# Kernel tuning notes

Measured on AMD Instinct MI355X. Metric: run time of the kernel, lower is better.

Reference implementation:

```python
import jax, jax.numpy as jnp
import numpy as np

N_NODES = 100000
DROP_P = 0.1


def gcn_conv(x, W, b, row, col, n_nodes):
    """PyG GCNConv: out = D^{-1/2}(A+I)D^{-1/2} X W + b.
    row/col already include self-loops. Messages flow row(src) -> col(dst)."""
    xw = x @ W  # [N, H]
    deg = jax.ops.segment_sum(jnp.ones_like(col, dtype=xw.dtype), col, num_segments=n_nodes)
    dinv = jnp.where(deg > 0, jax.lax.rsqrt(deg), 0.0)
    norm = dinv[row] * dinv[col]  # [E]
    msg = norm[:, None] * xw[row]  # [E, H] gather + scale
    out = jax.ops.segment_sum(msg, col, num_segments=n_nodes)  # scatter-add
    return out + b


def dropout(x, key, p):
    keep = jax.random.bernoulli(key, 1.0 - p, x.shape)
    return jnp.where(keep, x / (1.0 - p), 0.0).astype(x.dtype)


def prelu(x, alpha):
    return jnp.where(x >= 0, x, alpha[None, :] * x)


def setup_inputs() -> dict:
    key = jax.random.key(0)
    k1, k2, k3, k4 = jax.random.split(key, 4)
    in_ch, hid = 128, 128
    n_edges = 1600000
    x = jax.random.normal(k1, (N_NODES, in_ch), dtype=jnp.float32)
    edge_index = jax.random.randint(k2, (2, n_edges), 0, N_NODES, dtype=jnp.int64)
    s = 1.0 / np.sqrt(in_ch)
    W1 = jax.random.normal(k3, (in_ch, hid), dtype=jnp.float32) * s
    W2 = jax.random.normal(k4, (hid, hid), dtype=jnp.float32) * s
    b1 = jnp.zeros((hid,), dtype=jnp.float32)
    b2 = jnp.zeros((hid,), dtype=jnp.float32)
    alpha = jnp.full((hid,), 0.25, dtype=jnp.float32)
    return {"x": x, "edge_index": edge_index, "W1": W1, "b1": b1,
            "W2": W2, "b2": b2, "alpha": alpha}


def reference(x, edge_index, W1, b1, W2, b2, alpha):
    n = x.shape[0]
    # add self-loops once (PyG default add_self_loops=True)
    loop = jnp.arange(n, dtype=edge_index.dtype)
    row = jnp.concatenate([edge_index[0], loop])
    col = jnp.concatenate([edge_index[1], loop])

    dk1, dk2 = jax.random.split(jax.random.key(42))
    h = gcn_conv(x, W1, b1, row, col, n)
    h = dropout(h, dk1, DROP_P)
    h = prelu(h, alpha)
    h = gcn_conv(h, W2, b2, row, col, n)
    h = dropout(h, dk2, DROP_P)
    h = prelu(h, alpha)
    return h
```

## Files before the change

kernel.cpp:

```cpp
#include <hip/hip_runtime.h>
#include <stdint.h>
#include <string.h>

__host__ __device__ inline uint32_t rotl32(uint32_t x, int r) {
    return (x << r) | (x >> (32 - r));
}

__host__ __device__ inline void tf2x32(uint32_t k0, uint32_t k1,
                                       uint32_t x0, uint32_t x1,
                                       uint32_t& o0, uint32_t& o1) {
    uint32_t ks0 = k0, ks1 = k1, ks2 = k0 ^ k1 ^ 0x1BD11BDAu;
    x0 += ks0; x1 += ks1;
#define TF_R4(a,b,c,d) \
    x0 += x1; x1 = rotl32(x1,a); x1 ^= x0; \
    x0 += x1; x1 = rotl32(x1,b); x1 ^= x0; \
    x0 += x1; x1 = rotl32(x1,c); x1 ^= x0; \
    x0 += x1; x1 = rotl32(x1,d); x1 ^= x0;
    TF_R4(13,15,26,6)  x0 += ks1; x1 += ks2 + 1u;
    TF_R4(17,29,16,24) x0 += ks2; x1 += ks0 + 2u;
    TF_R4(13,15,26,6)  x0 += ks0; x1 += ks1 + 3u;
    TF_R4(17,29,16,24) x0 += ks1; x1 += ks2 + 4u;
    TF_R4(13,15,26,6)  x0 += ks2; x1 += ks0 + 5u;
#undef TF_R4
    o0 = x0; o1 = x1;
}

__device__ inline unsigned pk2h(float a, float b) {
    _Float16 ha = (_Float16)a, hb = (_Float16)b;
    unsigned short ua, ub;
    __builtin_memcpy(&ua, &ha, 2);
    __builtin_memcpy(&ub, &hb, 2);
    return (unsigned)ua | ((unsigned)ub << 16);
}
__device__ inline unsigned short h16bits(float a) {
    _Float16 h = (_Float16)a;
    unsigned short u; __builtin_memcpy(&u, &h, 2);
    return u;
}
__device__ inline float lo16(unsigned u) {
    unsigned short s = (unsigned short)(u & 0xffffu);
    _Float16 h; __builtin_memcpy(&h, &s, 2);
    return (float)h;
}
__device__ inline float hi16(unsigned u) {
    unsigned short s = (unsigned short)(u >> 16);
    _Float16 h; __builtin_memcpy(&h, &s, 2);
    return (float)h;
}

typedef float fx4 __attribute__((ext_vector_type(4)));
typedef unsigned ux4 __attribute__((ext_vector_type(4)));
typedef _Float16 h16x8 __attribute__((ext_vector_type(8)));
typedef _Float16 h16x2 __attribute__((ext_vector_type(2)));
typedef float f32x4 __attribute__((ext_vector_type(4)));

__device__ inline h16x2 as_h2(unsigned u) { h16x2 r; __builtin_memcpy(&r, &u, 4); return r; }

#define CSR_CAP 48
#define NBKT 256
#define PART_EPB 8192

__global__ __launch_bounds__(256) void k_part(
        const int* __restrict__ ei, long long* __restrict__ gbkt,
        unsigned* __restrict__ gbcnt,
        unsigned long long* __restrict__ m1, unsigned long long* __restrict__ m2,
        const float* __restrict__ x, unsigned* __restrict__ xb,
        const float* __restrict__ w1, const float* __restrict__ w2,
        _Float16* __restrict__ wt1, _Float16* __restrict__ wt2,
        unsigned k1a, unsigned k1b, unsigned k2a, unsigned k2b,
        int E, int N, int bw, int bcap, int total,
        int PB, int MB, int CB) {
    __shared__ unsigned hcnt[NBKT], hoff[NBKT], hrun[NBKT];
    int b = blockIdx.x;
    int t = (int)threadIdx.x;
    if (b < PB) {
        int base = b * PART_EPB;
        hcnt[t] = 0; hrun[t] = 0;
        __syncthreads();
        for (int i = 0; i < PART_EPB / 256; ++i) {
            int e = base + i * 256 + t;
            if (e < E) {
                int c = __builtin_nontemporal_load(ei + (size_t)E + e);
                int r = __builtin_nontemporal_load(ei + e);
                if ((unsigned)c < (unsigned)N && (unsigned)r < (unsigned)N)
                    atomicAdd(&hcnt[(unsigned)c / (unsigned)bw], 1u);
            }
        }
        __syncthreads();
        hoff[t] = atomicAdd(&gbcnt[t], hcnt[t]);
        __syncthreads();
        for (int i = 0; i < PART_EPB / 256; ++i) {
            int e = base + i * 256 + t;
            if (e < E) {
                int c = ei[(size_t)E + e];
                int r = ei[e];
                if ((unsigned)c < (unsigned)N && (unsigned)r < (unsigned)N) {
                    unsigned sp = (unsigned)c / (unsigned)bw;
                    unsigned rank = atomicAdd(&hrun[sp], 1u);
                    unsigned gp = hoff[sp] + rank;
                    if (gp < (unsigned)bcap)
                        gbkt[(size_t)sp * bcap + gp] =
                            (long long)(unsigned)r | ((long long)(unsigned)c << 32);
                }
            }
        }
        return;
    }
    b -= PB;
    if (b < MB) {
        int wv = (b * 256 + t) >> 6;
        int lane = t & 63;
        int TW = (2 * total) >> 6;
        int half = total >> 6;
        int w0 = wv * 8;
#pragma unroll
        for (int j = 0; j < 8; j++) {
            int wd = w0 + j;
            if (wd < TW) {
                int wl = wd;
                unsigned ka = k1a, kb = k1b;
                unsigned long long* m = m1;
                if (wl >= half) { wl -= half; ka = k2a; kb = k2b; m = m2; }
                uint32_t o0, o1;
                tf2x32(ka, kb, 0u, (uint32_t)(wl * 64 + lane), o0, o1);
                bool keep = (((o0 ^ o1) >> 9) < 7549747u);
                unsigned long long bal = __ballot(keep);
                if (lane == 0)
                    __builtin_nontemporal_store(bal, m + wl);
            }
        }
        return;
    }
    b -= MB;
    if (b < CB) {
        int i = b * 256 + t;
        if (i < (total >> 3)) {
            const fx4* src = (const fx4*)(x + (size_t)i * 8);
            fx4 a = __builtin_nontemporal_load(src);
            fx4 bb = __builtin_nontemporal_load(src + 1);
            ux4 v;
            v.x = pk2h(a.x, a.y);
            v.y = pk2h(a.z, a.w);
            v.z = pk2h(bb.x, bb.y);
            v.w = pk2h(bb.z, bb.w);
            __builtin_nontemporal_store(v, (ux4*)xb + i);
        }
        return;
    }
    b -= CB;
    int idx = b * 256 + t;
    int mat = idx >> 14;
    int e2 = idx & 16383;
    int c = e2 >> 7, k = e2 & 127;
    const float* W = mat ? w2 : w1;
    _Float16* WT = mat ? wt2 : wt1;
    WT[(size_t)c * 128 + k] = (_Float16)W[(size_t)k * 128 + c];
}

__global__ __launch_bounds__(256) void k_work(
        const long long* __restrict__ gbkt, const unsigned* __restrict__ gbcnt,
        unsigned* __restrict__ cnt, unsigned* __restrict__ csr,
        float* __restrict__ dinv, uint4* __restrict__ xb4,
        int N, int bw, int bcap) {
    __shared__ unsigned lcnt[512];
    int b = blockIdx.x;
    int t = (int)threadIdx.x;
    int lo = b * bw;
    int hi = lo + bw; if (hi > N) hi = N;
    int w = hi - lo; if (w < 0) w = 0;
    lcnt[t] = 0; lcnt[t + 256] = 0;
    __syncthreads();
    unsigned ne = gbcnt[b];
    if (ne > (unsigned)bcap) ne = (unsigned)bcap;
    const long long* base = gbkt + (size_t)b * bcap;
    for (unsigned e = t; e < ne; e += 256) {
        long long v = __builtin_nontemporal_load(base + e);
        unsigned r = (unsigned)(v & 0xffffffffll);
        unsigned c = (unsigned)(v >> 32);
        unsigned slot = atomicAdd(&lcnt[c - (unsigned)lo], 1u);
        if (slot < (unsigned)CSR_CAP)
            csr[(size_t)c * CSR_CAP + slot] = r;
    }
    __syncthreads();
    for (int i = t; i < w; i += 256)
        cnt[lo + i] = lcnt[i];
    for (int idx = t; idx < w * 16; idx += 256) {
        int nl = idx >> 4, part = idx & 15;
        int node = lo + nl;
        float d = rsqrtf((float)lcnt[nl] + 1.0f);
        if (part == 0) dinv[node] = d;
        uint4 u = xb4[(size_t)node * 16 + part];
        uint4 o;
        o.x = pk2h(d * lo16(u.x), d * hi16(u.x));
        o.y = pk2h(d * lo16(u.y), d * hi16(u.y));
        o.z = pk2h(d * lo16(u.z), d * hi16(u.z));
        o.w = pk2h(d * lo16(u.w), d * hi16(u.w));
        xb4[(size_t)node * 16 + part] = o;
    }
}

template <int OUT_HALF>
__global__ __launch_bounds__(128, 8) void k_layer(
        const unsigned short* __restrict__ in,
        const _Float16* __restrict__ WT,
        const float* __restrict__ bias, const float* __restrict__ alpha,
        const unsigned long long* __restrict__ mask,
        const float* __restrict__ dinv, const unsigned* __restrict__ cnt,
        const unsigned* __restrict__ csr,
        void* outv, int n) {
    __shared__ unsigned hls[32 * 68];
    int t = (int)threadIdx.x;
    int wv = t >> 6;
    int l = t & 63;
    int rowbase = blockIdx.x * 32 + wv * 16;
    unsigned* hl = hls + wv * 16 * 68;
    int slot = l >> 4;
    int lm = l & 15;
    int ci = lm << 3;

    int prow = rowbase + lm;
    bool pv = prow < n;
    float dnAll = pv ? dinv[prow] : 0.f;
    unsigned cAll = pv ? cnt[prow] : 0u;
    if (cAll > (unsigned)CSR_CAP) cAll = (unsigned)CSR_CAP;

#pragma unroll
    for (int g = 0; g < 4; ++g) {
        int rloc = g * 4 + slot;
        int node = rowbase + rloc;
        float dn = __shfl(dnAll, rloc);
        unsigned ecnt = (unsigned)__shfl((int)cAll, rloc);
        h16x2 a0 = (h16x2)0, a1 = (h16x2)0, a2 = (h16x2)0, a3 = (h16x2)0;
        size_t eb = (size_t)node * CSR_CAP;
        unsigned e = 0;
        unsigned nb4 = ecnt >> 2;
#pragma unroll 2
        for (unsigned bb = 0; bb < nb4; ++bb) {
            ux4 rr = __builtin_nontemporal_load((const ux4*)(csr + eb + e));
            uint4 u0 = *(const uint4*)(in + ((size_t)rr.x << 7) + ci);
            uint4 u1 = *(const uint4*)(in + ((size_t)rr.y << 7) + ci);
            uint4 u2 = *(const uint4*)(in + ((size_t)rr.z << 7) + ci);
            uint4 u3 = *(const uint4*)(in + ((size_t)rr.w << 7) + ci);
            a0 += as_h2(u0.x); a1 += as_h2(u0.y); a2 += as_h2(u0.z); a3 += as_h2(u0.w);
            a0 += as_h2(u1.x); a1 += as_h2(u1.y); a2 += as_h2(u1.z); a3 += as_h2(u1.w);
            a0 += as_h2(u2.x); a1 += as_h2(u2.y); a2 += as_h2(u2.z); a3 += as_h2(u2.w);
            a0 += as_h2(u3.x); a1 += as_h2(u3.y); a2 += as_h2(u3.z); a3 += as_h2(u3.w);
            e += 4;
        }
        for (; e < ecnt; ++e) {
            unsigned r0 = csr[eb + e];
            uint4 u0 = *(const uint4*)(in + ((size_t)r0 << 7) + ci);
            a0 += as_h2(u0.x); a1 += as_h2(u0.y); a2 += as_h2(u0.z); a3 += as_h2(u0.w);
        }
        if (node < n) {
            uint4 sv = *(const uint4*)(in + ((size_t)node << 7) + ci);
            a0 += as_h2(sv.x); a1 += as_h2(sv.y); a2 += as_h2(sv.z); a3 += as_h2(sv.w);
        }
        uint4 o;
        o.x = pk2h(dn * (float)a0[0], dn * (float)a0[1]);
        o.y = pk2h(dn * (float)a1[0], dn * (float)a1[1]);
        o.z = pk2h(dn * (float)a2[0], dn * (float)a2[1]);
        o.w = pk2h(dn * (float)a3[0], dn * (float)a3[1]);
        *(uint4*)(hl + (size_t)rloc * 68 + lm * 4) = o;
    }

    int kq = l >> 4;
    h16x8 afr[4];
#pragma unroll
    for (int kk = 0; kk < 4; kk++)
        afr[kk] = *(const h16x8*)(hl + (size_t)lm * 68 + kq * 4 + kk * 16);
#pragma unroll
    for (int f = 0; f < 8; f++) {
        f32x4 acc = (f32x4){0.f, 0.f, 0.f, 0.f};
#pragma unroll
        for (int kk = 0; kk < 4; kk++) {
            h16x8 bfr = *(const h16x8*)(WT + (size_t)(f * 16 + lm) * 128 + kk * 32 + kq * 8);
            acc = __builtin_amdgcn_mfma_f32_16x16x32_f16(afr[kk], bfr, acc, 0, 0, 0);
        }
        int c = f * 16 + lm;
        float bs = bias[c];
        float al = alpha[c];
#pragma unroll
        for (int j = 0; j < 4; j++) {
            int rl = kq * 4 + j;
            int rg = rowbase + rl;
            if (rg < n) {
                unsigned long long wmw = mask[((size_t)rg << 1) + (f >> 2)];
                bool keep = (wmw >> (c & 63)) & 1ull;
                float v = acc[j] + bs;
                v = keep ? v * (1.0f / 0.9f) : 0.0f;
                v = (v >= 0.f) ? v : al * v;
                if (OUT_HALF) {
                    float dnrow = __shfl(dnAll, rl);
                    __builtin_nontemporal_store(h16bits(v * dnrow),
                        (unsigned short*)outv + (size_t)rg * 128 + c);
                } else {
                    __builtin_nontemporal_store(v,
                        (float*)outv + (size_t)rg * 128 + c);
                }
            }
        }
    }
}

extern "C" void kernel_launch(void* const* d_in, const int* in_sizes, int n_in,
                              void* d_out, int out_size, void* d_ws, size_t ws_size,
                              hipStream_t stream) {
    const float* x  = (const float*)d_in[0];
    const int*   ei = (const int*)d_in[1];
    const float* W1 = (const float*)d_in[2];
    const float* b1 = (const float*)d_in[3];
    const float* W2 = (const float*)d_in[4];
    const float* b2 = (const float*)d_in[5];
    const float* al = (const float*)d_in[6];
    int N = in_sizes[0] / 128;
    int E = in_sizes[1] / 2;
    float* out = (float*)d_out;

    int bw = (N + NBKT - 1) / NBKT;
    int bcap = E / NBKT + E / NBKT / 4 + 1024;

    char* p = (char*)d_ws;
    unsigned short* xb = (unsigned short*)p;   p += (size_t)N * 128 * 2;
    unsigned short* ab = (unsigned short*)p;   p += (size_t)N * 128 * 2;
    long long* gbkt = (long long*)ab;
    unsigned* cnt = (unsigned*)p;              p += (size_t)N * 4;
    float* dinv = (float*)p;                   p += (size_t)N * 4;
    unsigned* csr = (unsigned*)p;              p += (size_t)N * CSR_CAP * 4;
    unsigned long long* m1 = (unsigned long long*)p;  p += ((size_t)N * 128 / 64) * 8;
    unsigned long long* m2 = (unsigned long long*)p;  p += ((size_t)N * 128 / 64) * 8;
    _Float16* wt1 = (_Float16*)p;              p += 128 * 128 * 2;
    _Float16* wt2 = (_Float16*)p;              p += 128 * 128 * 2;
    unsigned* gbcnt = (unsigned*)p;

    hipMemsetAsync(gbcnt, 0, NBKT * 4, stream);

    uint32_t dk1a, dk1b, dk2a, dk2b;
    tf2x32(0u, 42u, 0u, 0u, dk1a, dk1b);
    tf2x32(0u, 42u, 0u, 1u, dk2a, dk2b);

    int total = N * 128;
    int PB = (E + PART_EPB - 1) / PART_EPB;
    int TW = (2 * total) / 64;
    int MB = (TW + 31) / 32;
    int CB = (total / 8 + 255) / 256;
    int WB = (2 * 128 * 128 + 255) / 256;
    k_part<<<PB + MB + CB + WB, 256, 0, stream>>>(ei, gbkt, gbcnt, m1, m2,
                                                  x, (unsigned*)xb,
                                                  W1, W2, wt1, wt2,
                                                  dk1a, dk1b, dk2a, dk2b,
                                                  E, N, bw, bcap, total,
                                                  PB, MB, CB);
    k_work<<<NBKT, 256, 0, stream>>>(gbkt, gbcnt, cnt, csr, dinv, (uint4*)xb,
                                     N, bw, bcap);

    int LB = (N + 31) / 32;
    k_layer<1><<<LB, 128, 0, stream>>>(xb, wt1, b1, al, m1, dinv, cnt, csr, ab, N);
    k_layer<0><<<LB, 128, 0, stream>>>(ab, wt2, b2, al, m2, dinv, cnt, csr, out, N);
}
```

Measured before the change: 299.4 us.

## Split feature channels across both waves per 16-row block in layer kernel

Each block now handles 16 rows instead of 32, and its two waves split the 128 channels in half. Each lane gathers 8-byte chunks instead of 16-byte ones, and each wave computes 4 of the 8 MFMA output column tiles after a block-wide barrier. The change doubles the grid size and spreads the gather work across more blocks, which may improve latency hiding and load balance. In exchange, every CSR index is read twice (once per wave), the gather loads are narrower, and a __syncthreads is added.

Result: slower. 317.0 us (+5.9%).

```diff
diff --git a/kernel.cpp b/kernel.cpp
--- a/kernel.cpp
+++ b/kernel.cpp
@@ -208,15 +208,14 @@
         const float* __restrict__ dinv, const unsigned* __restrict__ cnt,
         const unsigned* __restrict__ csr,
         void* outv, int n) {
-    __shared__ unsigned hls[32 * 68];
+    __shared__ unsigned hl[16 * 68];
     int t = (int)threadIdx.x;
     int wv = t >> 6;
     int l = t & 63;
-    int rowbase = blockIdx.x * 32 + wv * 16;
-    unsigned* hl = hls + wv * 16 * 68;
+    int rowbase = blockIdx.x * 16;
     int slot = l >> 4;
     int lm = l & 15;
-    int ci = lm << 3;
+    int ch = wv * 64 + lm * 4;
 
     int prow = rowbase + lm;
     bool pv = prow < n;
@@ -230,39 +229,39 @@
         int node = rowbase + rloc;
         float dn = __shfl(dnAll, rloc);
         unsigned ecnt = (unsigned)__shfl((int)cAll, rloc);
-        h16x2 a0 = (h16x2)0, a1 = (h16x2)0, a2 = (h16x2)0, a3 = (h16x2)0;
+        h16x2 a0 = (h16x2)0, a1 = (h16x2)0;
         size_t eb = (size_t)node * CSR_CAP;
         unsigned e = 0;
         unsigned nb4 = ecnt >> 2;
 #pragma unroll 2
         for (unsigned bb = 0; bb < nb4; ++bb) {
             ux4 rr = __builtin_nontemporal_load((const ux4*)(csr + eb + e));
-            uint4 u0 = *(const uint4*)(in + ((size_t)rr.x << 7) + ci);
-            uint4 u1 = *(const uint4*)(in + ((size_t)rr.y << 7) + ci);
-            uint4 u2 = *(const uint4*)(in + ((size_t)rr.z << 7) + ci);
-            uint4 u3 = *(const uint4*)(in + ((size_t)rr.w << 7) + ci);
-            a0 += as_h2(u0.x); a1 += as_h2(u0.y); a2 += as_h2(u0.z); a3 += as_h2(u0.w);
-            a0 += as_h2(u1.x); a1 += as_h2(u1.y); a2 += as_h2(u1.z); a3 += as_h2(u1.w);
-            a0 += as_h2(u2.x); a1 += as_h2(u2.y); a2 += as_h2(u2.z); a3 += as_h2(u2.w);
-            a0 += as_h2(u3.x); a1 += as_h2(u3.y); a2 += as_h2(u3.z); a3 += as_h2(u3.w);
+            uint2 u0 = *(const uint2*)(in + ((size_t)rr.x << 7) + ch);
+            uint2 u1 = *(const uint2*)(in + ((size_t)rr.y << 7) + ch);
+            uint2 u2 = *(const uint2*)(in + ((size_t)rr.z << 7) + ch);
+            uint2 u3 = *(const uint2*)(in + ((size_t)rr.w << 7) + ch);
+            a0 += as_h2(u0.x); a1 += as_h2(u0.y);
+            a0 += as_h2(u1.x); a1 += as_h2(u1.y);
+            a0 += as_h2(u2.x); a1 += as_h2(u2.y);
+            a0 += as_h2(u3.x); a1 += as_h2(u3.y);
             e += 4;
         }
         for (; e < ecnt; ++e) {
             unsigned r0 = csr[eb + e];
-            uint4 u0 = *(const uint4*)(in + ((size_t)r0 << 7) + ci);
-            a0 += as_h2(u0.x); a1 += as_h2(u0.y); a2 += as_h2(u0.z); a3 += as_h2(u0.w);
+            uint2 u0 = *(const uint2*)(in + ((size_t)r0 << 7) + ch);
+            a0 += as_h2(u0.x); a1 += as_h2(u0.y);
         }
         if (node < n) {
-            uint4 sv = *(const uint4*)(in + ((size_t)node << 7) + ci);
-            a0 += as_h2(sv.x); a1 += as_h2(sv.y); a2 += as_h2(sv.z); a3 += as_h2(sv.w);
-        }
-        uint4 o;
+            uint2 sv = *(const uint2*)(in + ((size_t)node << 7) + ch);
+            a0 += as_h2(sv.x); a1 += as_h2(sv.y);
+        }
+        uint2 o;
         o.x = pk2h(dn * (float)a0[0], dn * (float)a0[1]);
         o.y = pk2h(dn * (float)a1[0], dn * (float)a1[1]);
-        o.z = pk2h(dn * (float)a2[0], dn * (float)a2[1]);
-        o.w = pk2h(dn * (float)a3[0], dn * (float)a3[1]);
-        *(uint4*)(hl + (size_t)rloc * 68 + lm * 4) = o;
-    }
+        *(uint2*)(hl + (size_t)rloc * 68 + wv * 32 + lm * 2) = o;
+    }
+
+    __syncthreads();
 
     int kq = l >> 4;
     h16x8 afr[4];
@@ -270,7 +269,8 @@
     for (int kk = 0; kk < 4; kk++)
         afr[kk] = *(const h16x8*)(hl + (size_t)lm * 68 + kq * 4 + kk * 16);
 #pragma unroll
-    for (int f = 0; f < 8; f++) {
+    for (int fi = 0; fi < 4; fi++) {
+        int f = wv * 4 + fi;
         f32x4 acc = (f32x4){0.f, 0.f, 0.f, 0.f};
 #pragma unroll
         for (int kk = 0; kk < 4; kk++) {
@@ -285,7 +285,7 @@
             int rl = kq * 4 + j;
             int rg = rowbase + rl;
             if (rg < n) {
-                unsigned long long wmw = mask[((size_t)rg << 1) + (f >> 2)];
+                unsigned long long wmw = mask[((size_t)rg << 1) + wv];
                 bool keep = (wmw >> (c & 63)) & 1ull;
                 float v = acc[j] + bs;
                 v = keep ? v * (1.0f / 0.9f) : 0.0f;
@@ -354,7 +354,7 @@
     k_work<<<NBKT, 256, 0, stream>>>(gbkt, gbcnt, cnt, csr, dinv, (uint4*)xb,
                                      N, bw, bcap);
 
-    int LB = (N + 31) / 32;
+    int LB = (N + 15) / 16;
     k_layer<1><<<LB, 128, 0, stream>>>(xb, wt1, b1, al, m1, dinv, cnt, csr, ab, N);
     k_layer<0><<<LB, 128, 0, stream>>>(ab, wt2, b2, al, m2, dinv, cnt, csr, out, N);
 }
```
